# Performance work log

Hardware: AMD Instinct MI355X
Metric: run time of the kernel (lower is better)

## Reference

```python
import jax, jax.numpy as jnp
import numpy as np

B, N, D, H, I = 16, 1024, 1024, 16, 4096
HS = D // H  # 64
EPS = 1e-5


def setup_inputs() -> dict:
    key = jax.random.key(0)
    ks = jax.random.split(key, 8)
    w = lambda k, shape: (jax.random.normal(k, shape, jnp.float32) * 0.02)
    return {
        'hidden_states': jax.random.normal(ks[0], (B, N, D), jnp.float32),
        'ln1_g': jnp.ones((D,), jnp.float32), 'ln1_b': jnp.zeros((D,), jnp.float32),
        'ln2_g': jnp.ones((D,), jnp.float32), 'ln2_b': jnp.zeros((D,), jnp.float32),
        'wq': w(ks[1], (D, D)), 'bq': jnp.zeros((D,), jnp.float32),
        'wk': w(ks[2], (D, D)), 'bk': jnp.zeros((D,), jnp.float32),
        'wv': w(ks[3], (D, D)), 'bv': jnp.zeros((D,), jnp.float32),
        'w1': w(ks[4], (D, I)), 'b1': jnp.zeros((I,), jnp.float32),
        'w2': w(ks[5], (I, D)), 'b2': jnp.zeros((D,), jnp.float32),
    }


def _layernorm(x, g, b):
    m = jnp.mean(x, axis=-1, keepdims=True)
    v = jnp.var(x, axis=-1, keepdims=True)
    return (x - m) * jax.lax.rsqrt(v + EPS) * g + b


def _split_heads(t):
    # Faithful to transpose_for_scores: reshape (B,N,HS,H) -> (B,H,N,HS)
    # i.e. head h takes the strided feature slice t[..., h::H].
    b, n, _ = t.shape
    return t.reshape(b, n, HS, H).transpose(0, 3, 1, 2)


def _vit_layer(x, ln1_g, ln1_b, ln2_g, ln2_b, wq, bq, wk, bk, wv, bv, w1, b1, w2, b2):
    h = _layernorm(x, ln1_g, ln1_b)
    q = _split_heads(h @ wq + bq)  # [B,H,N,HS]
    k = _split_heads(h @ wk + bk)
    v = _split_heads(h @ wv + bv)
    scores = jax.nn.softmax(jnp.einsum('bhqd,bhkd->bhqk', q, k) / np.sqrt(HS).astype(np.float32), axis=-1)
    attn = jnp.einsum('bhqk,bhkd->bhqd', scores, v)          # [B,H,N,HS]
    attn = attn.transpose(0, 2, 1, 3).reshape(x.shape)       # head-major merge (as in source)
    x = x + attn
    h = _layernorm(x, ln2_g, ln2_b)
    mlp = jax.nn.silu(h @ w1 + b1) @ w2 + b2
    return x + mlp


def reference(hidden_states, ln1_g, ln1_b, ln2_g, ln2_b, wq, bq, wk, bk, wv, bv, w1, b1, w2, b2):
    return _vit_layer(hidden_states, ln1_g, ln1_b, ln2_g, ln2_b, wq, bq, wk, bk, wv, bv, w1, b1, w2, b2)
```

## Files before the change

kernel.cpp:

```cpp
#include <hip/hip_runtime.h>
#include <hip/hip_bf16.h>
#include <stdint.h>

typedef __bf16 bf16;
typedef bf16 bf16x8 __attribute__((ext_vector_type(8)));
typedef bf16 bf16x4 __attribute__((ext_vector_type(4)));
typedef float f32x4 __attribute__((ext_vector_type(4)));

static __device__ __forceinline__ f32x4 mfma16(bf16x8 a, bf16x8 b, f32x4 c) {
    return __builtin_amdgcn_mfma_f32_16x16x32_bf16(a, b, c, 0, 0, 0);
}

static __device__ __forceinline__ void gld16(const bf16* g, bf16* l) {
    __builtin_amdgcn_global_load_lds((const __attribute__((address_space(1))) void*)g,
                                     (__attribute__((address_space(3))) void*)l, 16, 0, 0);
}

static __device__ __forceinline__ uint32_t pkbf(float a, float b) {
    union { bf16 h[2]; uint32_t u; } u_;
    u_.h[0] = (bf16)a; u_.h[1] = (bf16)b;
    return u_.u;
}

static __device__ __forceinline__ void xcd_supertile(int gdx, int gdy,
                                                     int& bx, int& by) {
    const int orig = blockIdx.y * gdx + blockIdx.x;
    const int xcd = orig & 7;
    const int idx = orig >> 3;
    const int CBY = gdy >> 3;
    const int gx = (gdx >= 4) ? 4 : gdx;
    const int gy = (CBY >= 4) ? 4 : CBY;
    const int cells = gx * gy;
    const int st = idx / cells, off = idx % cells;
    const int nstx = gdx / gx;
    const int stx = st % nstx, sty = st / nstx;
    bx = stx * gx + off % gx;
    by = xcd * CBY + sty * gy + off / gx;
}

static __device__ __forceinline__ void tcast_body_p1(
    const float* __restrict__ src, bf16* __restrict__ dst,
    int R, int C, int bx, int by, int tid, float (*t)[33]) {
    const int tx = tid & 31, ty = tid >> 5;
    const int c0 = bx * 32, r0 = by * 32;
#pragma unroll
    for (int j = 0; j < 4; ++j)
        t[ty + j * 8][tx] = src[(size_t)(r0 + ty + j * 8) * C + c0 + tx];
    __syncthreads();
#pragma unroll
    for (int j = 0; j < 4; ++j) {
        const int c = c0 + ty + j * 8;
        const int cp = ((c & 15) << 6) | (c >> 4);
        dst[(size_t)cp * R + r0 + tx] = (bf16)t[tx][ty + j * 8];
    }
}

static __device__ __forceinline__ void tcast_body_p0(
    const float* __restrict__ src, bf16* __restrict__ dst,
    int R, int C, int bx, int by, int tid, float (*t)[33]) {
    const int tx = tid & 31, ty = tid >> 5;
    const int c0 = bx * 32, r0 = by * 32;
#pragma unroll
    for (int j = 0; j < 4; ++j)
        t[ty + j * 8][tx] = src[(size_t)(r0 + ty + j * 8) * C + c0 + tx];
    __syncthreads();
#pragma unroll
    for (int j = 0; j < 4; ++j) {
        const int c = c0 + ty + j * 8;
        dst[(size_t)c * R + r0 + tx] = (bf16)t[tx][ty + j * 8];
    }
}

__global__ __launch_bounds__(256)
void prologue_kernel(const float* __restrict__ wq, const float* __restrict__ wk,
                     const float* __restrict__ wv, const float* __restrict__ w1,
                     const float* __restrict__ w2,
                     const float* __restrict__ bq, const float* __restrict__ bk,
                     const float* __restrict__ bv,
                     const float* __restrict__ x, const float* __restrict__ gg,
                     const float* __restrict__ bb,
                     bf16* __restrict__ Wqkvt, bf16* __restrict__ W1t,
                     bf16* __restrict__ W2t, float* __restrict__ bqkvp,
                     bf16* __restrict__ Xln) {
    __shared__ float t[32][33];
    __shared__ float red[8];
    const int blk = blockIdx.x, tid = threadIdx.x;

    if (blk < 3072) {
        const int seg = blk >> 10, b = blk & 1023;
        const float* src = (seg == 0) ? wq : (seg == 1) ? wk : wv;
        tcast_body_p1(src, Wqkvt + (size_t)seg * 1024 * 1024,
                      1024, 1024, b & 31, b >> 5, tid, t);
    } else if (blk < 7168) {
        const int b = blk - 3072;
        tcast_body_p0(w1, W1t, 1024, 4096, b & 127, b >> 7, tid, t);
    } else if (blk < 11264) {
        const int b = blk - 7168;
        tcast_body_p0(w2, W2t, 4096, 1024, b & 31, b >> 5, tid, t);
    } else if (blk < 11276) {
        const int i = (blk - 11264) * 256 + tid;
        const int seg = i >> 10, c = i & 1023;
        const int src = ((c & 63) << 4) | (c >> 6);
        const float* b = (seg == 0) ? bq : (seg == 1) ? bk : bv;
        bqkvp[i] = b[src];
    } else {
        const int row = blk - 11276;
        const int lane = tid & 63, wid = tid >> 6;
        const float4 v = ((const float4*)(x + (size_t)row * 1024))[tid];
        float s  = v.x + v.y + v.z + v.w;
        float s2 = v.x * v.x + v.y * v.y + v.z * v.z + v.w * v.w;
#pragma unroll
        for (int m = 1; m <= 32; m <<= 1) {
            s  += __shfl_xor(s,  m);
            s2 += __shfl_xor(s2, m);
        }
        if (lane == 0) { red[wid] = s; red[wid + 4] = s2; }
        __syncthreads();
        float ts  = red[0] + red[1] + red[2] + red[3];
        float ts2 = red[4] + red[5] + red[6] + red[7];
        float mean = ts * (1.f / 1024.f);
        float var  = ts2 * (1.f / 1024.f) - mean * mean;
        float rs   = rsqrtf(var + 1e-5f);
        const float4 gv = ((const float4*)gg)[tid];
        const float4 bv4 = ((const float4*)bb)[tid];
        bf16x4 o;
        o[0] = (bf16)((v.x - mean) * rs * gv.x + bv4.x);
        o[1] = (bf16)((v.y - mean) * rs * gv.y + bv4.y);
        o[2] = (bf16)((v.z - mean) * rs * gv.z + bv4.z);
        o[3] = (bf16)((v.w - mean) * rs * gv.w + bv4.w);
        *(bf16x4*)(Xln + (size_t)row * 1024 + tid * 4) = o;
    }
}

__global__ __launch_bounds__(256)
void ln_bf_kernel(const bf16* __restrict__ x, const float* __restrict__ gg,
                  const float* __restrict__ bb, bf16* __restrict__ out) {
    __shared__ float red[8];
    const int row = blockIdx.x, tid = threadIdx.x;
    const int lane = tid & 63, wid = tid >> 6;
    const bf16x4 vb = *(const bf16x4*)(x + (size_t)row * 1024 + tid * 4);
    const float v0 = (float)vb[0], v1 = (float)vb[1];
    const float v2 = (float)vb[2], v3 = (float)vb[3];
    float s  = v0 + v1 + v2 + v3;
    float s2 = v0 * v0 + v1 * v1 + v2 * v2 + v3 * v3;
#pragma unroll
    for (int m = 1; m <= 32; m <<= 1) {
        s  += __shfl_xor(s,  m);
        s2 += __shfl_xor(s2, m);
    }
    if (lane == 0) { red[wid] = s; red[wid + 4] = s2; }
    __syncthreads();
    float ts  = red[0] + red[1] + red[2] + red[3];
    float ts2 = red[4] + red[5] + red[6] + red[7];
    float mean = ts * (1.f / 1024.f);
    float var  = ts2 * (1.f / 1024.f) - mean * mean;
    float rs   = rsqrtf(var + 1e-5f);
    const float4 gv = ((const float4*)gg)[tid];
    const float4 bv = ((const float4*)bb)[tid];
    bf16x4 o;
    o[0] = (bf16)((v0 - mean) * rs * gv.x + bv.x);
    o[1] = (bf16)((v1 - mean) * rs * gv.y + bv.y);
    o[2] = (bf16)((v2 - mean) * rs * gv.z + bv.z);
    o[3] = (bf16)((v3 - mean) * rs * gv.w + bv.w);
    *(bf16x4*)(out + (size_t)row * 1024 + tid * 4) = o;
}

template <int MODE>
__global__ __launch_bounds__(512, 2)
void gemm256(const bf16* __restrict__ A, const bf16* __restrict__ Bt,
             int M, int N, int K,
             const float* __restrict__ bias_a,
             const bf16* __restrict__ resid, float* __restrict__ outF,
             bf16* __restrict__ oB,
             bf16* __restrict__ oQ, bf16* __restrict__ oK, bf16* __restrict__ oV) {
    __shared__ alignas(16) bf16 As[2][256 * 64];
    __shared__ alignas(16) bf16 Bs[2][256 * 64];
    const int tid = threadIdx.x;
    const int wid = tid >> 6, lane = tid & 63;
    const int li = lane & 15, g = lane >> 4;
    const int wm = wid >> 2, wn = wid & 3;

    int bx, by;
    xcd_supertile(gridDim.x, gridDim.y, bx, by);
    const int row0 = by * 256, col0 = bx * 256;

    const int gsrc = ((tid & 7) ^ ((tid >> 3) & 7)) << 3;
    const bf16* gA = A + (size_t)(row0 + (tid >> 3)) * K + gsrc;
    const bf16* gB = Bt + (size_t)(col0 + (tid >> 3)) * K + gsrc;

    f32x4 acc[8][4] = {};
    const int nt = K >> 6;

    const int ro0 = (((0 * 4 + g) ^ (li & 7)) << 3);
    const int ro1 = (((1 * 4 + g) ^ (li & 7)) << 3);

#pragma unroll
    for (int j = 0; j < 4; ++j) {
        gld16(gA + (size_t)(64 * j) * K, &As[0][j * 4096 + (wid << 9)]);
        gld16(gB + (size_t)(64 * j) * K, &Bs[0][j * 4096 + (wid << 9)]);
    }

#define RDA(dst, p)                                                        \
    do {                                                                   \
        _Pragma("unroll")                                                  \
        for (int ii = 0; ii < 2; ++ii) {                                   \
            const int rr = wm * 128 + ((p) * 2 + ii) * 16 + li;            \
            dst[ii][0] = *(const bf16x8*)(At + rr * 64 + ro0);             \
            dst[ii][1] = *(const bf16x8*)(At + rr * 64 + ro1);             \
        }                                                                  \
    } while (0)

#define MFMAP(p, src)                                                      \
    do {                                                                   \
        __builtin_amdgcn_s_setprio(1);                                     \
        _Pragma("unroll")                                                  \
        for (int ii = 0; ii < 2; ++ii)                                     \
            _Pragma("unroll")                                              \
            for (int jf = 0; jf < 4; ++jf) {                               \
                acc[(p) * 2 + ii][jf] = mfma16(src[ii][0], bfr[jf][0],     \
                                               acc[(p) * 2 + ii][jf]);     \
                acc[(p) * 2 + ii][jf] = mfma16(src[ii][1], bfr[jf][1],     \
                                               acc[(p) * 2 + ii][jf]);     \
            }                                                              \
        __builtin_amdgcn_s_setprio(0);                                     \
    } while (0)

    for (int t = 0; t < nt; ++t) {
        asm volatile("s_waitcnt vmcnt(0)" ::: "memory");
        __builtin_amdgcn_s_barrier();
        __builtin_amdgcn_sched_barrier(0);

        const bf16* At = &As[t & 1][0];
        const bf16* Bl = &Bs[t & 1][0];
        bf16* Asn = &As[(t & 1) ^ 1][0];
        bf16* Bsn = &Bs[(t & 1) ^ 1][0];
        const bool pf = (t + 1 < nt);
        const size_t koff = (size_t)(t + 1) << 6;

        bf16x8 bfr[4][2];
#pragma unroll
        for (int jf = 0; jf < 4; ++jf) {
            const int rb = wn * 64 + jf * 16 + li;
            bfr[jf][0] = *(const bf16x8*)(Bl + rb * 64 + ro0);
            bfr[jf][1] = *(const bf16x8*)(Bl + rb * 64 + ro1);
        }
        bf16x8 afA[2][2], afB[2][2];
        RDA(afA, 0);
        if (pf) {
            gld16(gB + koff,                   Bsn + (wid << 9));
            gld16(gB + (size_t)64 * K + koff,  Bsn + 4096 + (wid << 9));
            gld16(gB + (size_t)128 * K + koff, Bsn + 2 * 4096 + (wid << 9));
            gld16(gB + (size_t)192 * K + koff, Bsn + 3 * 4096 + (wid << 9));
        }
        RDA(afB, 1);
        asm volatile("s_waitcnt lgkmcnt(4)" ::: "memory");
        __builtin_amdgcn_sched_barrier(0);
        MFMAP(0, afA);

        RDA(afA, 2);
        asm volatile("s_waitcnt lgkmcnt(4)" ::: "memory");
        __builtin_amdgcn_sched_barrier(0);
        MFMAP(1, afB);

        if (pf) {
            gld16(gA + koff,                   Asn + (wid << 9));
            gld16(gA + (size_t)64 * K + koff,  Asn + 4096 + (wid << 9));
            gld16(gA + (size_t)128 * K + koff, Asn + 2 * 4096 + (wid << 9));
            gld16(gA + (size_t)192 * K + koff, Asn + 3 * 4096 + (wid << 9));
        }
        RDA(afB, 3);
        asm volatile("s_waitcnt lgkmcnt(4)" ::: "memory");
        __builtin_amdgcn_sched_barrier(0);
        MFMAP(2, afA);

        asm volatile("s_waitcnt lgkmcnt(0)" ::: "memory");
        __builtin_amdgcn_sched_barrier(0);
        MFMAP(3, afB);
    }
#undef RDA
#undef MFMAP

    if (MODE == 0) {
        __builtin_amdgcn_s_barrier();
        const int seg = col0 >> 10;
        const int h   = ((col0 & 1023) >> 6) + wn;
        const int bb  = row0 >> 10;
        const int n0  = (row0 & 1023) + wm * 128;
        float bias[4];
#pragma unroll
        for (int jf = 0; jf < 4; ++jf) bias[jf] = bias_a[col0 + wn * 64 + jf * 16 + li];

        if (seg == 2) {
#pragma unroll
            for (int i = 0; i < 8; ++i)
#pragma unroll
                for (int jf = 0; jf < 4; ++jf) {
                    const int d = jf * 16 + li;
                    bf16x4 pv;
#pragma unroll
                    for (int r = 0; r < 4; ++r) pv[r] = (bf16)(acc[i][jf][r] + bias[jf]);
                    *(bf16x4*)(oV + ((size_t)(bb * 16 + h) * 64 + d) * 1024
                                   + n0 + i * 16 + g * 4) = pv;
                }
        } else {
            char* ep = (wid < 4) ? ((char*)&As[0][0] + wid * 16384)
                                 : ((char*)&Bs[0][0] + (wid - 4) * 16384);
            const float scale = (seg == 0) ? 0.18033688f : 1.0f;
            bf16* og = (seg == 0) ? oQ : oK;
#pragma unroll
            for (int i = 0; i < 8; ++i)
#pragma unroll
                for (int jf = 0; jf < 4; ++jf)
#pragma unroll
                    for (int r = 0; r < 4; ++r) {
                        const int rr = i * 16 + g * 4 + r;
                        const int byte = (rr * 128 + (jf * 16 + li) * 2) ^ ((rr & 7) << 4);
                        *(bf16*)(ep + byte) = (bf16)((acc[i][jf][r] + bias[jf]) * scale);
                    }
            bf16* gb = og + ((size_t)(bb * 16 + h) * 1024 + n0) * 64;
#pragma unroll
            for (int tt = 0; tt < 16; ++tt) {
                const int rr = tt * 8 + (lane >> 3);
                const int d0 = (lane & 7) * 8;
                const int byte = (rr * 128 + d0 * 2) ^ ((rr & 7) << 4);
                bf16x8 val = *(const bf16x8*)(ep + byte);
                *(bf16x8*)(gb + (size_t)rr * 64 + d0) = val;
            }
        }
        return;
    }

#pragma unroll
    for (int i = 0; i < 8; ++i) {
        const int row = row0 + wm * 128 + i * 16 + g * 4;
#pragma unroll
        for (int jf = 0; jf < 4; ++jf) {
            const int col = col0 + wn * 64 + jf * 16 + li;
            const float bias = bias_a[col];
            if (MODE == 1) {
#pragma unroll
                for (int r = 0; r < 4; ++r) {
                    float val = acc[i][jf][r] + bias;
                    val = val / (1.f + __expf(-val));
                    oB[(size_t)(row + r) * N + col] = (bf16)val;
                }
            } else {
#pragma unroll
                for (int r = 0; r < 4; ++r) {
                    const size_t idx = (size_t)(row + r) * N + col;
                    outF[idx] = acc[i][jf][r] + bias + (float)resid[idx];
                }
            }
        }
    }
}

__global__ __launch_bounds__(256)
void attn_kernel(const bf16* __restrict__ Q, const bf16* __restrict__ Kb,
                 const bf16* __restrict__ Vt, const float* __restrict__ x,
                 bf16* __restrict__ out) {
    __shared__ alignas(16) bf16 Kl[2][4096];
    __shared__ alignas(16) bf16 Vl[2][4096];
    __shared__ alignas(16) char Ps[4][4096];
    const int tid = threadIdx.x, wid = tid >> 6, lane = tid & 63;
    const int li = lane & 15, g = lane >> 4;
    const int bid = blockIdx.x;
    const int bh = (bid & 7) + ((bid >> 6) << 3);
    const int qt = (bid >> 3) & 7;
    const int b = bh >> 4, h = bh & 15;
    const size_t base = (size_t)bh << 16;
    const bf16* Qp = Q + base + (size_t)(qt * 128 + wid * 32) * 64;
    const bf16* Kp = Kb + base;
    const bf16* Vp = Vt + base;
    char* psw = Ps[wid];
    const int swz = (li & 7) << 4;

    const int srow = lane >> 3;
    const int sslot = (lane & 7) ^ srow;

    bf16x8 aq[2][2];
#pragma unroll
    for (int fr = 0; fr < 2; ++fr)
#pragma unroll
        for (int ks = 0; ks < 2; ++ks)
            aq[fr][ks] = *(const bf16x8*)(Qp + (fr * 16 + li) * 64 + ks * 32 + g * 8);

#pragma unroll
    for (int hh = 0; hh < 2; ++hh) {
        const int r = wid * 16 + hh * 8 + srow;
        gld16(Kp + (size_t)r * 64 + sslot * 8, &Kl[0][(wid * 16 + hh * 8) * 64]);
        gld16(Vp + (size_t)r * 1024 + sslot * 8, &Vl[0][(wid * 16 + hh * 8) * 64]);
    }
    asm volatile("s_waitcnt vmcnt(0)" ::: "memory");
    __builtin_amdgcn_s_barrier();

    f32x4 o[2][4] = {};
    float lacc[2] = {0.f, 0.f};

    for (int kt = 0; kt < 16; ++kt) {
        const int cur = kt & 1;
        const bf16* Kt = Kl[cur];
        const bf16* Vtl = Vl[cur];
        if (kt < 15) {
            const int nb = (kt + 1) * 64;
#pragma unroll
            for (int hh = 0; hh < 2; ++hh) {
                const int r = wid * 16 + hh * 8 + srow;
                gld16(Kp + (size_t)(nb + r) * 64 + sslot * 8,
                      &Kl[cur ^ 1][(wid * 16 + hh * 8) * 64]);
                gld16(Vp + (size_t)r * 1024 + nb + sslot * 8,
                      &Vl[cur ^ 1][(wid * 16 + hh * 8) * 64]);
            }
            asm volatile("s_waitcnt vmcnt(4)" ::: "memory");
        } else {
            asm volatile("s_waitcnt vmcnt(0)" ::: "memory");
        }
        __builtin_amdgcn_s_barrier();
        __builtin_amdgcn_sched_barrier(0);

        f32x4 s[2][4] = {};
        __builtin_amdgcn_s_setprio(1);
#pragma unroll
        for (int jc = 0; jc < 4; ++jc) {
            const int row = jc * 16 + li;
#pragma unroll
            for (int ks = 0; ks < 2; ++ks) {
                bf16x8 kf = *(const bf16x8*)(Kt + row * 64 + (((ks * 4 + g) ^ (li & 7)) * 8));
                s[0][jc] = mfma16(kf, aq[0][ks], s[0][jc]);
                s[1][jc] = mfma16(kf, aq[1][ks], s[1][jc]);
            }
        }
        __builtin_amdgcn_s_setprio(0);

#pragma unroll
        for (int fr = 0; fr < 2; ++fr) {
            float pj[4];
#pragma unroll
            for (int jc = 0; jc < 4; ++jc) {
#pragma unroll
                for (int r = 0; r < 4; ++r)
                    s[fr][jc][r] = exp2f(s[fr][jc][r]);
                pj[jc] = (s[fr][jc][0] + s[fr][jc][1]) + (s[fr][jc][2] + s[fr][jc][3]);
            }
            lacc[fr] += (pj[0] + pj[1]) + (pj[2] + pj[3]);

            const int qb = (fr * 16 + li) * 128;
#pragma unroll
            for (int jc = 0; jc < 4; ++jc) {
                uint2 w;
                w.x = pkbf(s[fr][jc][0], s[fr][jc][1]);
                w.y = pkbf(s[fr][jc][2], s[fr][jc][3]);
                *(uint2*)(psw + ((qb + jc * 32 + g * 8) ^ swz)) = w;
            }
        }

#pragma unroll
        for (int ks2 = 0; ks2 < 2; ++ks2) {
            bf16x8 pa0 = *(const bf16x8*)(psw + ((li * 128 + ks2 * 64 + g * 16) ^ swz));
            bf16x8 pa1 = *(const bf16x8*)(psw + (((16 + li) * 128 + ks2 * 64 + g * 16) ^ swz));
            __builtin_amdgcn_s_setprio(1);
#pragma unroll
            for (int jd = 0; jd < 4; ++jd) {
                const int row = jd * 16 + li;
                bf16x8 vf = *(const bf16x8*)(Vtl + row * 64 + (((ks2 * 4 + g) ^ (li & 7)) * 8));
                o[0][jd] = mfma16(vf, pa0, o[0][jd]);
                o[1][jd] = mfma16(vf, pa1, o[1][jd]);
            }
            __builtin_amdgcn_s_setprio(0);
        }
        __builtin_amdgcn_sched_barrier(0);
        __builtin_amdgcn_s_barrier();
    }

    float lrun[2];
#pragma unroll
    for (int fr = 0; fr < 2; ++fr) {
        float l = lacc[fr];
        l += __shfl_xor(l, 16);
        l += __shfl_xor(l, 32);
        lrun[fr] = l;
    }

    const int n0 = qt * 128 + wid * 32;
#pragma unroll
    for (int fr = 0; fr < 2; ++fr) {
        const float inv = 1.f / lrun[fr];
        const int n = n0 + fr * 16 + li;
        const size_t rowb = (size_t)(b * 1024 + n) * 1024 + h * 64;
#pragma unroll
        for (int jd = 0; jd < 4; ++jd) {
            const int c = jd * 16 + g * 4;
            const float4 xv = *(const float4*)(x + rowb + c);
            bf16x4 ov;
            ov[0] = (bf16)(xv.x + o[fr][jd][0] * inv);
            ov[1] = (bf16)(xv.y + o[fr][jd][1] * inv);
            ov[2] = (bf16)(xv.z + o[fr][jd][2] * inv);
            ov[3] = (bf16)(xv.w + o[fr][jd][3] * inv);
            *(bf16x4*)(out + rowb + c) = ov;
        }
    }
}

extern "C" void kernel_launch(void* const* d_in, const int* in_sizes, int n_in,
                              void* d_out, int out_size, void* d_ws, size_t ws_size,
                              hipStream_t stream) {
    const float* x    = (const float*)d_in[0];
    const float* ln1g = (const float*)d_in[1];
    const float* ln1b = (const float*)d_in[2];
    const float* ln2g = (const float*)d_in[3];
    const float* ln2b = (const float*)d_in[4];
    const float* wq   = (const float*)d_in[5];
    const float* bq   = (const float*)d_in[6];
    const float* wk   = (const float*)d_in[7];
    const float* bk   = (const float*)d_in[8];
    const float* wv   = (const float*)d_in[9];
    const float* bv   = (const float*)d_in[10];
    const float* w1   = (const float*)d_in[11];
    const float* b1   = (const float*)d_in[12];
    const float* w2   = (const float*)d_in[13];
    const float* b2   = (const float*)d_in[14];

    char* ws = (char*)d_ws;
    const size_t MB = 1024 * 1024;
    bf16*  Wqkvt  = (bf16*)(ws);
    bf16*  W1t    = (bf16*)(ws + 6 * MB);
    bf16*  W2t    = (bf16*)(ws + 14 * MB);
    bf16*  aresb  = (bf16*)(ws + 22 * MB);
    bf16*  Xln    = (bf16*)(ws + 86 * MB);
    bf16*  Qb     = (bf16*)(ws + 118 * MB);
    bf16*  Kbuf   = (bf16*)(ws + 150 * MB);
    bf16*  Vtb    = (bf16*)(ws + 182 * MB);
    bf16*  mid    = (bf16*)(ws + 118 * MB);
    float* bqkvp  = (float*)(ws + 245 * MB);

    prologue_kernel<<<27660, 256, 0, stream>>>(wq, wk, wv, w1, w2,
        bq, bk, bv, x, ln1g, ln1b, Wqkvt, W1t, W2t, bqkvp, Xln);

    gemm256<0><<<dim3(12, 64), 512, 0, stream>>>(Xln, Wqkvt, 16384, 3072, 1024,
        bqkvp, nullptr, nullptr, nullptr, Qb, Kbuf, Vtb);

    attn_kernel<<<2048, 256, 0, stream>>>(Qb, Kbuf, Vtb, x, aresb);

    ln_bf_kernel<<<16384, 256, 0, stream>>>(aresb, ln2g, ln2b, Xln);

    gemm256<1><<<dim3(16, 64), 512, 0, stream>>>(Xln, W1t, 16384, 4096, 1024,
        b1, nullptr, nullptr, mid, nullptr, nullptr, nullptr);

    gemm256<2><<<dim3(4, 64), 512, 0, stream>>>(mid, W2t, 16384, 1024, 4096,
        b2, aresb, (float*)d_out, nullptr, nullptr, nullptr, nullptr);
}
```

Baseline: 613.9 us.

## Restructure GEMM main loop into quadrant phases with staggered prefetch and barriers

Replaces the per-tile single barrier and four-phase A-row loop with four quadrant phases (A half × B half), each doing its own LDS reads, issuing two async global-to-LDS prefetches, and bracketing its MFMAs with barriers. The prologue and prefetch order are staggered so only the chunks needed next are waited on (vmcnt(2)), letting the next tile's loads overlap with compute at finer granularity. The cost is more LDS fragment reads per tile and more barriers per iteration, and correctness depends on the vmcnt bookkeeping being exact.

```diff
diff --git a/kernel.cpp b/kernel.cpp
--- a/kernel.cpp
+++ b/kernel.cpp
@@ -194,42 +194,18 @@
     const int ro0 = (((0 * 4 + g) ^ (li & 7)) << 3);
     const int ro1 = (((1 * 4 + g) ^ (li & 7)) << 3);
 
-#pragma unroll
-    for (int j = 0; j < 4; ++j) {
-        gld16(gA + (size_t)(64 * j) * K, &As[0][j * 4096 + (wid << 9)]);
-        gld16(gB + (size_t)(64 * j) * K, &Bs[0][j * 4096 + (wid << 9)]);
-    }
-
-#define RDA(dst, p)                                                        \
-    do {                                                                   \
-        _Pragma("unroll")                                                  \
-        for (int ii = 0; ii < 2; ++ii) {                                   \
-            const int rr = wm * 128 + ((p) * 2 + ii) * 16 + li;            \
-            dst[ii][0] = *(const bf16x8*)(At + rr * 64 + ro0);             \
-            dst[ii][1] = *(const bf16x8*)(At + rr * 64 + ro1);             \
-        }                                                                  \
-    } while (0)
-
-#define MFMAP(p, src)                                                      \
-    do {                                                                   \
-        __builtin_amdgcn_s_setprio(1);                                     \
-        _Pragma("unroll")                                                  \
-        for (int ii = 0; ii < 2; ++ii)                                     \
-            _Pragma("unroll")                                              \
-            for (int jf = 0; jf < 4; ++jf) {                               \
-                acc[(p) * 2 + ii][jf] = mfma16(src[ii][0], bfr[jf][0],     \
-                                               acc[(p) * 2 + ii][jf]);     \
-                acc[(p) * 2 + ii][jf] = mfma16(src[ii][1], bfr[jf][1],     \
-                                               acc[(p) * 2 + ii][jf]);     \
-            }                                                              \
-        __builtin_amdgcn_s_setprio(0);                                     \
-    } while (0)
+    gld16(gA,                    &As[0][(wid << 9)]);
+    gld16(gA + (size_t)128 * K,  &As[0][2 * 4096 + (wid << 9)]);
+    gld16(gB,                    &Bs[0][(wid << 9)]);
+    gld16(gB + (size_t)64 * K,   &Bs[0][4096 + (wid << 9)]);
+    gld16(gB + (size_t)128 * K,  &Bs[0][2 * 4096 + (wid << 9)]);
+    gld16(gB + (size_t)192 * K,  &Bs[0][3 * 4096 + (wid << 9)]);
+    gld16(gA + (size_t)64 * K,   &As[0][4096 + (wid << 9)]);
+    gld16(gA + (size_t)192 * K,  &As[0][3 * 4096 + (wid << 9)]);
+    asm volatile("s_waitcnt vmcnt(2)" ::: "memory");
+    __builtin_amdgcn_s_barrier();
 
     for (int t = 0; t < nt; ++t) {
-        asm volatile("s_waitcnt vmcnt(0)" ::: "memory");
-        __builtin_amdgcn_s_barrier();
-        __builtin_amdgcn_sched_barrier(0);
-
         const bf16* At = &As[t & 1][0];
         const bf16* Bl = &Bs[t & 1][0];
         bf16* Asn = &As[(t & 1) ^ 1][0];
@@ -237,48 +213,60 @@
         const bool pf = (t + 1 < nt);
         const size_t koff = (size_t)(t + 1) << 6;
 
-        bf16x8 bfr[4][2];
-#pragma unroll
-        for (int jf = 0; jf < 4; ++jf) {
-            const int rb = wn * 64 + jf * 16 + li;
-            bfr[jf][0] = *(const bf16x8*)(Bl + rb * 64 + ro0);
-            bfr[jf][1] = *(const bf16x8*)(Bl + rb * 64 + ro1);
-        }
-        bf16x8 afA[2][2], afB[2][2];
-        RDA(afA, 0);
-        if (pf) {
-            gld16(gB + koff,                   Bsn + (wid << 9));
-            gld16(gB + (size_t)64 * K + koff,  Bsn + 4096 + (wid << 9));
-            gld16(gB + (size_t)128 * K + koff, Bsn + 2 * 4096 + (wid << 9));
-            gld16(gB + (size_t)192 * K + koff, Bsn + 3 * 4096 + (wid << 9));
-        }
-        RDA(afB, 1);
-        asm volatile("s_waitcnt lgkmcnt(4)" ::: "memory");
-        __builtin_amdgcn_sched_barrier(0);
-        MFMAP(0, afA);
-
-        RDA(afA, 2);
-        asm volatile("s_waitcnt lgkmcnt(4)" ::: "memory");
-        __builtin_amdgcn_sched_barrier(0);
-        MFMAP(1, afB);
-
-        if (pf) {
-            gld16(gA + koff,                   Asn + (wid << 9));
-            gld16(gA + (size_t)64 * K + koff,  Asn + 4096 + (wid << 9));
-            gld16(gA + (size_t)128 * K + koff, Asn + 2 * 4096 + (wid << 9));
-            gld16(gA + (size_t)192 * K + koff, Asn + 3 * 4096 + (wid << 9));
-        }
-        RDA(afB, 3);
-        asm volatile("s_waitcnt lgkmcnt(4)" ::: "memory");
-        __builtin_amdgcn_sched_barrier(0);
-        MFMAP(2, afA);
-
-        asm volatile("s_waitcnt lgkmcnt(0)" ::: "memory");
-        __builtin_amdgcn_sched_barrier(0);
-        MFMAP(3, afB);
-    }
-#undef RDA
-#undef MFMAP
+#pragma unroll
+        for (int p = 0; p < 4; ++p) {
+            const int qa = p & 1, qb = p >> 1;
+            bf16x8 af[4][2], bfr[2][2];
+#pragma unroll
+            for (int ii = 0; ii < 4; ++ii) {
+                const int rr = wm * 128 + qa * 64 + ii * 16 + li;
+                af[ii][0] = *(const bf16x8*)(At + rr * 64 + ro0);
+                af[ii][1] = *(const bf16x8*)(At + rr * 64 + ro1);
+            }
+#pragma unroll
+            for (int jj = 0; jj < 2; ++jj) {
+                const int rb = wn * 64 + qb * 32 + jj * 16 + li;
+                bfr[jj][0] = *(const bf16x8*)(Bl + rb * 64 + ro0);
+                bfr[jj][1] = *(const bf16x8*)(Bl + rb * 64 + ro1);
+            }
+            if (pf) {
+                if (p == 0) {
+                    gld16(gA + koff,                   Asn + (wid << 9));
+                    gld16(gA + (size_t)128 * K + koff, Asn + 2 * 4096 + (wid << 9));
+                } else if (p == 1) {
+                    gld16(gB + koff,                   Bsn + (wid << 9));
+                    gld16(gB + (size_t)64 * K + koff,  Bsn + 4096 + (wid << 9));
+                } else if (p == 2) {
+                    gld16(gB + (size_t)128 * K + koff, Bsn + 2 * 4096 + (wid << 9));
+                    gld16(gB + (size_t)192 * K + koff, Bsn + 3 * 4096 + (wid << 9));
+                } else {
+                    gld16(gA + (size_t)64 * K + koff,  Asn + 4096 + (wid << 9));
+                    gld16(gA + (size_t)192 * K + koff, Asn + 3 * 4096 + (wid << 9));
+                }
+            }
+            __builtin_amdgcn_s_barrier();
+            asm volatile("s_waitcnt lgkmcnt(0)" ::: "memory");
+            __builtin_amdgcn_sched_barrier(0);
+            __builtin_amdgcn_s_setprio(1);
+#pragma unroll
+            for (int ii = 0; ii < 4; ++ii)
+#pragma unroll
+                for (int jj = 0; jj < 2; ++jj) {
+                    const int ai = qa * 4 + ii, bj = qb * 2 + jj;
+                    acc[ai][bj] = mfma16(af[ii][0], bfr[jj][0], acc[ai][bj]);
+                    acc[ai][bj] = mfma16(af[ii][1], bfr[jj][1], acc[ai][bj]);
+                }
+            __builtin_amdgcn_s_setprio(0);
+            __builtin_amdgcn_sched_barrier(0);
+            if (p == 0) {
+                if (pf) asm volatile("s_waitcnt vmcnt(2)" ::: "memory");
+                else    asm volatile("s_waitcnt vmcnt(0)" ::: "memory");
+            }
+            if (p == 3 && pf)
+                asm volatile("s_waitcnt vmcnt(2)" ::: "memory");
+            __builtin_amdgcn_s_barrier();
+        }
+    }
 
     if (MODE == 0) {
         __builtin_amdgcn_s_barrier();
```

After: 653.2 us. 1.06x slower.
